# Performance work log

Hardware: AMD Instinct MI355X
Metric: run time of the kernel (lower is better)

## Reference

```python
import jax, jax.numpy as jnp
import numpy as np
from jax import lax


def _cubic(A, B, C, D, x):
    # A..D: [B,C,H,W]; x: [B,H,W] fractional coordinate, broadcast over channels
    x = x[:, None, :, :]
    return B + 0.5 * x * (C - A + x * (2.0 * A - 5.0 * B + 4.0 * C - D
                                       + x * (3.0 * (B - C) + D - A)))


def _bicubic(im, grid):
    Bn, Cc, H, W = im.shape
    gx = grid[0, 0]  # [H,W]
    gy = grid[0, 1]
    x0 = jnp.floor(gx - 1.0).astype(jnp.int32)
    y0 = jnp.floor(gy - 1.0).astype(jnp.int32)
    x3 = x0 + 3
    y3 = y0 + 3
    outside = (x0 < 0) | (x3 > W - 1) | (y0 < 0) | (y3 > H - 1)
    mask = jnp.where(outside, 0.0, 1.0).astype(im.dtype)[None, None]
    mask = jnp.broadcast_to(mask, im.shape)
    xs = [jnp.clip(x0 + k, 0, W - 1) for k in range(4)]
    ys = [jnp.clip(y0 + k, 0, H - 1) for k in range(4)]
    ty = grid[:, 1] - jnp.floor(grid[:, 1])  # frac along y, used in inner cubic
    tx = grid[:, 0] - jnp.floor(grid[:, 0])  # frac along x, used in outer cubic
    cols = [_cubic(im[:, :, ys[0], xs[j]], im[:, :, ys[1], xs[j]],
                   im[:, :, ys[2], xs[j]], im[:, :, ys[3], xs[j]], ty)
            for j in range(4)]
    out = _cubic(cols[0], cols[1], cols[2], cols[3], tx)
    return out, mask


def _warp(x, flo):
    Bn, Cc, H, W = x.shape
    xx = jnp.broadcast_to(jnp.arange(W, dtype=flo.dtype)[None, :], (H, W))
    yy = jnp.broadcast_to(jnp.arange(H, dtype=flo.dtype)[:, None], (H, W))
    base = jnp.stack([xx, yy], axis=0)[None]  # [1,2,H,W]
    vgrid = base + flo
    return _bicubic(x, vgrid)


def _occlusion_mask(of, old_mask):
    Bn, Cc, H, W = old_mask.shape
    a = jnp.zeros((H, W), of.dtype).at[:-1, :].set(of[0, 0, 1:, :] - of[0, 0, :-1, :])
    b = jnp.zeros((H, W), of.dtype).at[:, :-1].set(of[0, 1, :, 1:] - of[0, 1, :, :-1])
    m = (jnp.abs(a + b) > 0.75).astype(of.dtype)
    # binary dilation with a 4x4 ones structuring element == max-pool 4x4
    m = lax.reduce_window(m, 0.0, lax.max, (4, 4), (1, 1), ((1, 2), (1, 2)))
    m = (m.at[0:2, :].set(1.0).at[H - 2:H, :].set(1.0)
          .at[:, 0:2].set(1.0).at[:, W - 2:W].set(1.0))
    return old_mask * (1.0 - m)[None, None]


def setup_inputs() -> dict:
    key = jax.random.key(0)
    ks = jax.random.split(key, 7)
    B, C, H, W = 1, 3, 1080, 1920
    return {
        "input1": jax.random.normal(ks[0], (B, C, H, W), jnp.float32),
        "input2": jax.random.normal(ks[1], (B, C, H, W), jnp.float32),
        "prev_frame1": jax.random.normal(ks[2], (C, H, W), jnp.float32),
        "flow1": jax.random.normal(ks[3], (B, 2, H, W), jnp.float32),
        "mask1_0": jax.random.uniform(ks[4], (B, C, H, W), jnp.float32),
        "exclusive_mask1": jax.random.uniform(ks[5], (B, C, H, W), jnp.float32),
        "fastdvdnet": jax.random.normal(ks[6], (B, C, H, W), jnp.float32),
    }


def reference(input1, input2, prev_frame1, flow1, mask1_0, exclusive_mask1, fastdvdnet):
    prev1 = prev_frame1[None]
    warped1, mask1 = _warp(input1, flow1)
    mask1 = _occlusion_mask(flow1, mask1)
    Mask1 = mask1_0 * mask1
    warp1, m1 = _warp(input2, flow1)
    m1 = _occlusion_mask(flow1, m1)
    wfast, m11 = _warp(fastdvdnet, flow1)
    m11 = _occlusion_mask(flow1, m11)
    m1 = m1 * m11
    l1 = jnp.mean(jnp.abs(exclusive_mask1 * Mask1 * warped1
                          - exclusive_mask1 * Mask1 * prev1))
    l2 = jnp.mean(jnp.abs(m1 * exclusive_mask1 * (1.0 - Mask1) * warp1
                          - m1 * exclusive_mask1 * (1.0 - Mask1) * wfast))
    return l1 + l2
```

## Files before the change

kernel.cpp:

```cpp
#include <hip/hip_runtime.h>


__device__ __forceinline__ void cr_weights(float t, float w[4]) {
    float t2 = t * t, t3 = t2 * t;
    w[0] = 0.5f * (-t + 2.0f * t2 - t3);
    w[1] = 1.0f + 0.5f * (3.0f * t3 - 5.0f * t2);
    w[2] = 0.5f * (t + 4.0f * t2 - 3.0f * t3);
    w[3] = 0.5f * (t3 - t2);
}

__device__ __forceinline__ float bicubic4(const float* __restrict__ p, int W,
                                          const float wx[4], const float wy[4]) {
    float s = 0.0f;
#pragma unroll
    for (int k = 0; k < 4; ++k) {
        const float* r = p + k * W;
        float h = wx[0] * r[0];
        h = fmaf(wx[1], r[1], h);
        h = fmaf(wx[2], r[2], h);
        h = fmaf(wx[3], r[3], h);
        s = fmaf(wy[k], h, s);
    }
    return s;
}

__global__ void occl_hpool_kernel(const float* __restrict__ flow,
                                  unsigned char* __restrict__ mh,
                                  double* __restrict__ acc, int H, int W) {
    int idx = blockIdx.x * blockDim.x + threadIdx.x;
    if (idx == 0) acc[0] = 0.0;
    int HW = H * W;
    if (idx >= HW) return;
    int y = idx / W;
    int x = idx - y * W;
    const float* __restrict__ f0 = flow;
    const float* __restrict__ f1 = flow + HW;
    bool have_a = (y < H - 1);
    int m = 0;
#pragma unroll
    for (int dx = -1; dx <= 2; ++dx) {
        int xx = x + dx;
        if (xx < 0 || xx >= W) continue;
        float a = have_a ? (f0[(y + 1) * W + xx] - f0[y * W + xx]) : 0.0f;
        float b = (xx < W - 1) ? (f1[y * W + xx + 1] - f1[y * W + xx]) : 0.0f;
        m |= (fabsf(a + b) > 0.75f) ? 1 : 0;
    }
    mh[idx] = (unsigned char)m;
}

__global__ void zero_acc_kernel(double* __restrict__ acc) { acc[0] = 0.0; }

template <bool INLINE_OCC>
__global__ void loss_kernel(const float* __restrict__ in1,
                            const float* __restrict__ in2,
                            const float* __restrict__ prev,
                            const float* __restrict__ flow,
                            const float* __restrict__ m10,
                            const float* __restrict__ ex,
                            const float* __restrict__ fast,
                            const unsigned char* __restrict__ mh,
                            double* __restrict__ acc, int H, int W) {
    int idx = blockIdx.x * blockDim.x + threadIdx.x;
    int HW = H * W;
    float local = 0.0f;
    if (idx < HW) {
        int y = idx / W;
        int x = idx - y * W;
        int occ;
        if (y < 2 || y >= H - 2 || x < 2 || x >= W - 2) {
            occ = 1;
        } else if (INLINE_OCC) {
            occ = 0;
            const float* __restrict__ f0 = flow;
            const float* __restrict__ f1 = flow + HW;
            for (int dy = -1; dy <= 2; ++dy) {
                int yy = y + dy;
                for (int dx = -1; dx <= 2; ++dx) {
                    int xx = x + dx;
                    float a = (yy < H - 1) ? (f0[(yy + 1) * W + xx] - f0[yy * W + xx]) : 0.0f;
                    float b = (xx < W - 1) ? (f1[yy * W + xx + 1] - f1[yy * W + xx]) : 0.0f;
                    occ |= (fabsf(a + b) > 0.75f) ? 1 : 0;
                }
            }
        } else {
            occ = 0;
#pragma unroll
            for (int dy = -1; dy <= 2; ++dy) occ |= mh[(y + dy) * W + x];
        }

        if (!occ) {
            float fx = flow[idx];
            float fy = flow[HW + idx];
            float gx = (float)x + fx;
            float gy = (float)y + fy;
            float fgx = floorf(gx), fgy = floorf(gy);
            int x0 = (int)fgx - 1;
            int y0 = (int)fgy - 1;
            if (x0 >= 0 && x0 <= W - 4 && y0 >= 0 && y0 <= H - 4) {
                float tx = gx - fgx, ty = gy - fgy;
                float wx[4], wy[4];
                cr_weights(tx, wx);
                cr_weights(ty, wy);
                size_t base = (size_t)y0 * W + x0;
#pragma unroll
                for (int c = 0; c < 3; ++c) {
                    size_t coff = (size_t)c * HW;
                    float w1 = bicubic4(in1 + coff + base, W, wx, wy);
                    float w2 = bicubic4(in2 + coff + base, W, wx, wy);
                    float wf = bicubic4(fast + coff + base, W, wx, wy);
                    float M = m10[coff + idx];
                    float e = ex[coff + idx];
                    float t1 = fabsf(e * M * (w1 - prev[coff + idx]));
                    float t2 = fabsf(e * (1.0f - M) * (w2 - wf));
                    local += t1 + t2;
                }
            }
        }
    }

#pragma unroll
    for (int off = 32; off > 0; off >>= 1) local += __shfl_down(local, off, 64);
    __shared__ float wsum[4];
    int wid = threadIdx.x >> 6;
    if ((threadIdx.x & 63) == 0) wsum[wid] = local;
    __syncthreads();
    if (threadIdx.x == 0) {
        float s = wsum[0] + wsum[1] + wsum[2] + wsum[3];
        if (s != 0.0f) atomicAdd(acc, (double)s);
    }
}

__global__ void finalize_kernel(const double* __restrict__ acc,
                                float* __restrict__ out, double invN) {
    out[0] = (float)(acc[0] * invN);
}

extern "C" void kernel_launch(void* const* d_in, const int* in_sizes, int n_in,
                              void* d_out, int out_size, void* d_ws, size_t ws_size,
                              hipStream_t stream) {
    const float* in1  = (const float*)d_in[0];
    const float* in2  = (const float*)d_in[1];
    const float* prev = (const float*)d_in[2];
    const float* flow = (const float*)d_in[3];
    const float* m10  = (const float*)d_in[4];
    const float* ex   = (const float*)d_in[5];
    const float* fast = (const float*)d_in[6];
    float* out = (float*)d_out;

    const int H = 1080, W = 1920;
    const int HW = H * W;

    double* acc = (double*)d_ws;
    unsigned char* mh = (unsigned char*)d_ws + 64;

    const int threads = 256;
    const int blocks = (HW + threads - 1) / threads;
    const double invN = 1.0 / (3.0 * (double)HW);

    if (ws_size >= (size_t)HW + 64) {
        occl_hpool_kernel<<<blocks, threads, 0, stream>>>(flow, mh, acc, H, W);
        loss_kernel<false><<<blocks, threads, 0, stream>>>(in1, in2, prev, flow,
                                                           m10, ex, fast, mh, acc, H, W);
    } else {
        zero_acc_kernel<<<1, 1, 0, stream>>>(acc);
        loss_kernel<true><<<blocks, threads, 0, stream>>>(in1, in2, prev, flow,
                                                          m10, ex, fast, nullptr, acc, H, W);
    }
    finalize_kernel<<<1, 1, 0, stream>>>(acc, out, invN);
}
```

Measured before the change: 158.5 us.

## Fuse occlusion mask into loss kernel via shared-memory tiles and deterministic reduction

Replaces the separate horizontal-pool kernel and its global byte mask with a 2D-tiled fused kernel. Each 64x4 block computes the edge flags for its haloed tile in shared memory and pools them there. Per-block partial sums go to a workspace array and a single-block kernel reduces them, replacing the double-precision atomics and the finalize kernel. This removes one launch and a global mask round trip, at the cost of recomputing halo flags and adding two block barriers.

```diff
diff --git a/kernel.cpp b/kernel.cpp
--- a/kernel.cpp
+++ b/kernel.cpp
@@ -1,5 +1,16 @@
 #include <hip/hip_runtime.h>
 
+
+constexpr int HH = 1080, WW = 1920;
+constexpr int HW = HH * WW;
+constexpr int TLX = 64, TLY = 4;
+constexpr int RAW_C = TLX + 3;
+constexpr int RAW_R = TLY + 3;
+constexpr int NRAW = RAW_R * RAW_C;
+constexpr int NHP = RAW_R * TLX;
+constexpr int NBX = WW / TLX;
+constexpr int NBY = HH / TLY;
+constexpr int NB = NBX * NBY;
 
 __device__ __forceinline__ void cr_weights(float t, float w[4]) {
     float t2 = t * t, t3 = t2 * t;
@@ -9,12 +20,12 @@
     w[3] = 0.5f * (t3 - t2);
 }
 
-__device__ __forceinline__ float bicubic4(const float* __restrict__ p, int W,
+__device__ __forceinline__ float bicubic4(const float* __restrict__ p,
                                           const float wx[4], const float wy[4]) {
     float s = 0.0f;
 #pragma unroll
     for (int k = 0; k < 4; ++k) {
-        const float* r = p + k * W;
+        const float* r = p + k * WW;
         float h = wx[0] * r[0];
         h = fmaf(wx[1], r[1], h);
         h = fmaf(wx[2], r[2], h);
@@ -24,115 +35,96 @@
     return s;
 }
 
-__global__ void occl_hpool_kernel(const float* __restrict__ flow,
-                                  unsigned char* __restrict__ mh,
-                                  double* __restrict__ acc, int H, int W) {
-    int idx = blockIdx.x * blockDim.x + threadIdx.x;
-    if (idx == 0) acc[0] = 0.0;
-    int HW = H * W;
-    if (idx >= HW) return;
-    int y = idx / W;
-    int x = idx - y * W;
+__global__ __launch_bounds__(256) void fused_loss_kernel(
+    const float* __restrict__ in1, const float* __restrict__ in2,
+    const float* __restrict__ prev, const float* __restrict__ flow,
+    const float* __restrict__ m10, const float* __restrict__ ex,
+    const float* __restrict__ fast, float* __restrict__ partial) {
+    __shared__ unsigned char raw[RAW_R][RAW_C + 5];
+    __shared__ unsigned char hp[RAW_R][TLX];
+    __shared__ float wsum[4];
+
+    const int t = threadIdx.x;
+    const int x0 = blockIdx.x * TLX;
+    const int y0 = blockIdx.y * TLY;
     const float* __restrict__ f0 = flow;
     const float* __restrict__ f1 = flow + HW;
-    bool have_a = (y < H - 1);
-    int m = 0;
+
+    for (int e = t; e < NRAW; e += 256) {
+        int rr = e / RAW_C, cc = e - rr * RAW_C;
+        int yy = y0 - 1 + rr, xx = x0 - 1 + cc;
+        int flag = 0;
+        if (yy >= 0 && yy < HH && xx >= 0 && xx < WW) {
+            float a = (yy < HH - 1) ? f0[(yy + 1) * WW + xx] - f0[yy * WW + xx] : 0.0f;
+            float b = (xx < WW - 1) ? f1[yy * WW + xx + 1] - f1[yy * WW + xx] : 0.0f;
+            flag = (fabsf(a + b) > 0.75f) ? 1 : 0;
+        }
+        raw[rr][cc] = (unsigned char)flag;
+    }
+    __syncthreads();
+
+    for (int e = t; e < NHP; e += 256) {
+        int rr = e >> 6, cc = e & 63;
+        hp[rr][cc] = raw[rr][cc] | raw[rr][cc + 1] | raw[rr][cc + 2] | raw[rr][cc + 3];
+    }
+    __syncthreads();
+
+    const int tx = t & 63, ty = t >> 6;
+    const int x = x0 + tx, y = y0 + ty;
+    int occ = hp[ty][tx] | hp[ty + 1][tx] | hp[ty + 2][tx] | hp[ty + 3][tx];
+    if (y < 2 || y >= HH - 2 || x < 2 || x >= WW - 2) occ = 1;
+
+    float local = 0.0f;
+    if (!occ) {
+        int idx = y * WW + x;
+        float fx = flow[idx];
+        float fy = flow[HW + idx];
+        float gx = (float)x + fx;
+        float gy = (float)y + fy;
+        float fgx = floorf(gx), fgy = floorf(gy);
+        int bx0 = (int)fgx - 1;
+        int by0 = (int)fgy - 1;
+        if (bx0 >= 0 && bx0 <= WW - 4 && by0 >= 0 && by0 <= HH - 4) {
+            float txf = gx - fgx, tyf = gy - fgy;
+            float wxw[4], wyw[4];
+            cr_weights(txf, wxw);
+            cr_weights(tyf, wyw);
+            size_t base = (size_t)by0 * WW + bx0;
 #pragma unroll
-    for (int dx = -1; dx <= 2; ++dx) {
-        int xx = x + dx;
-        if (xx < 0 || xx >= W) continue;
-        float a = have_a ? (f0[(y + 1) * W + xx] - f0[y * W + xx]) : 0.0f;
-        float b = (xx < W - 1) ? (f1[y * W + xx + 1] - f1[y * W + xx]) : 0.0f;
-        m |= (fabsf(a + b) > 0.75f) ? 1 : 0;
-    }
-    mh[idx] = (unsigned char)m;
-}
-
-__global__ void zero_acc_kernel(double* __restrict__ acc) { acc[0] = 0.0; }
-
-template <bool INLINE_OCC>
-__global__ void loss_kernel(const float* __restrict__ in1,
-                            const float* __restrict__ in2,
-                            const float* __restrict__ prev,
-                            const float* __restrict__ flow,
-                            const float* __restrict__ m10,
-                            const float* __restrict__ ex,
-                            const float* __restrict__ fast,
-                            const unsigned char* __restrict__ mh,
-                            double* __restrict__ acc, int H, int W) {
-    int idx = blockIdx.x * blockDim.x + threadIdx.x;
-    int HW = H * W;
-    float local = 0.0f;
-    if (idx < HW) {
-        int y = idx / W;
-        int x = idx - y * W;
-        int occ;
-        if (y < 2 || y >= H - 2 || x < 2 || x >= W - 2) {
-            occ = 1;
-        } else if (INLINE_OCC) {
-            occ = 0;
-            const float* __restrict__ f0 = flow;
-            const float* __restrict__ f1 = flow + HW;
-            for (int dy = -1; dy <= 2; ++dy) {
-                int yy = y + dy;
-                for (int dx = -1; dx <= 2; ++dx) {
-                    int xx = x + dx;
-                    float a = (yy < H - 1) ? (f0[(yy + 1) * W + xx] - f0[yy * W + xx]) : 0.0f;
-                    float b = (xx < W - 1) ? (f1[yy * W + xx + 1] - f1[yy * W + xx]) : 0.0f;
-                    occ |= (fabsf(a + b) > 0.75f) ? 1 : 0;
-                }
-            }
-        } else {
-            occ = 0;
-#pragma unroll
-            for (int dy = -1; dy <= 2; ++dy) occ |= mh[(y + dy) * W + x];
-        }
-
-        if (!occ) {
-            float fx = flow[idx];
-            float fy = flow[HW + idx];
-            float gx = (float)x + fx;
-            float gy = (float)y + fy;
-            float fgx = floorf(gx), fgy = floorf(gy);
-            int x0 = (int)fgx - 1;
-            int y0 = (int)fgy - 1;
-            if (x0 >= 0 && x0 <= W - 4 && y0 >= 0 && y0 <= H - 4) {
-                float tx = gx - fgx, ty = gy - fgy;
-                float wx[4], wy[4];
-                cr_weights(tx, wx);
-                cr_weights(ty, wy);
-                size_t base = (size_t)y0 * W + x0;
-#pragma unroll
-                for (int c = 0; c < 3; ++c) {
-                    size_t coff = (size_t)c * HW;
-                    float w1 = bicubic4(in1 + coff + base, W, wx, wy);
-                    float w2 = bicubic4(in2 + coff + base, W, wx, wy);
-                    float wf = bicubic4(fast + coff + base, W, wx, wy);
-                    float M = m10[coff + idx];
-                    float e = ex[coff + idx];
-                    float t1 = fabsf(e * M * (w1 - prev[coff + idx]));
-                    float t2 = fabsf(e * (1.0f - M) * (w2 - wf));
-                    local += t1 + t2;
-                }
+            for (int c = 0; c < 3; ++c) {
+                size_t coff = (size_t)c * HW;
+                float w1 = bicubic4(in1 + coff + base, wxw, wyw);
+                float w2 = bicubic4(in2 + coff + base, wxw, wyw);
+                float wf = bicubic4(fast + coff + base, wxw, wyw);
+                float M = m10[coff + idx];
+                float e = ex[coff + idx];
+                local += fabsf(e * M * (w1 - prev[coff + idx]));
+                local += fabsf(e * (1.0f - M) * (w2 - wf));
             }
         }
     }
 
 #pragma unroll
     for (int off = 32; off > 0; off >>= 1) local += __shfl_down(local, off, 64);
-    __shared__ float wsum[4];
-    int wid = threadIdx.x >> 6;
-    if ((threadIdx.x & 63) == 0) wsum[wid] = local;
+    int wid = t >> 6;
+    if ((t & 63) == 0) wsum[wid] = local;
     __syncthreads();
-    if (threadIdx.x == 0) {
-        float s = wsum[0] + wsum[1] + wsum[2] + wsum[3];
-        if (s != 0.0f) atomicAdd(acc, (double)s);
-    }
+    if (t == 0)
+        partial[blockIdx.y * NBX + blockIdx.x] = wsum[0] + wsum[1] + wsum[2] + wsum[3];
 }
 
-__global__ void finalize_kernel(const double* __restrict__ acc,
-                                float* __restrict__ out, double invN) {
-    out[0] = (float)(acc[0] * invN);
+__global__ __launch_bounds__(256) void reduce_kernel(
+    const float* __restrict__ partial, float* __restrict__ out, double invN) {
+    double s = 0.0;
+    for (int i = threadIdx.x; i < NB; i += 256) s += (double)partial[i];
+#pragma unroll
+    for (int off = 32; off > 0; off >>= 1) s += __shfl_down(s, off, 64);
+    __shared__ double wsum[4];
+    int wid = threadIdx.x >> 6;
+    if ((threadIdx.x & 63) == 0) wsum[wid] = s;
+    __syncthreads();
+    if (threadIdx.x == 0)
+        out[0] = (float)((wsum[0] + wsum[1] + wsum[2] + wsum[3]) * invN);
 }
 
 extern "C" void kernel_launch(void* const* d_in, const int* in_sizes, int n_in,
@@ -147,24 +139,11 @@
     const float* fast = (const float*)d_in[6];
     float* out = (float*)d_out;
 
-    const int H = 1080, W = 1920;
-    const int HW = H * W;
-
-    double* acc = (double*)d_ws;
-    unsigned char* mh = (unsigned char*)d_ws + 64;
-
-    const int threads = 256;
-    const int blocks = (HW + threads - 1) / threads;
+    float* partial = (float*)d_ws;
     const double invN = 1.0 / (3.0 * (double)HW);
 
-    if (ws_size >= (size_t)HW + 64) {
-        occl_hpool_kernel<<<blocks, threads, 0, stream>>>(flow, mh, acc, H, W);
-        loss_kernel<false><<<blocks, threads, 0, stream>>>(in1, in2, prev, flow,
-                                                           m10, ex, fast, mh, acc, H, W);
-    } else {
-        zero_acc_kernel<<<1, 1, 0, stream>>>(acc);
-        loss_kernel<true><<<blocks, threads, 0, stream>>>(in1, in2, prev, flow,
-                                                          m10, ex, fast, nullptr, acc, H, W);
-    }
-    finalize_kernel<<<1, 1, 0, stream>>>(acc, out, invN);
+    dim3 grid(NBX, NBY);
+    fused_loss_kernel<<<grid, 256, 0, stream>>>(in1, in2, prev, flow, m10, ex,
+                                                fast, partial);
+    reduce_kernel<<<1, 256, 0, stream>>>(partial, out, invN);
 }
```

Measured after the change: 169.0 us. 6.6% more time.
